# Performance work log

Measured on AMD Instinct MI355X. Metric: run time of the kernel, lower is better.

Reference implementation:

```python
import jax, jax.numpy as jnp
import numpy as np

# dims: B batch, T timesteps, S sensors, O obs_dim, E obs_embed_dim, P pe_emb_dim, A inter-sensor attn dim
B, T, S, O, E, P, A, OUT = 64, 128, 64, 4, 64, 16, 10, 128


def positional_encoding(times, pe_dim):
    # standard sinusoidal PE over continuous times -> (B, T, pe_dim)
    # (sin block then cos block; mathematically same frequencies as interleaved torch version)
    freq = jnp.exp(jnp.arange(0, pe_dim, 2, dtype=jnp.float32) * (-jnp.log(10000.0) / pe_dim))
    ang = times[..., None] * freq  # (B, T, pe_dim//2)
    return jnp.concatenate([jnp.sin(ang), jnp.cos(ang)], axis=-1)


def setup_inputs() -> dict:
    key = jax.random.key(0)
    ks = jax.random.split(key, 16)
    x = jax.random.normal(ks[0], (B, T, S, O), dtype=jnp.float32)
    times = jnp.sort(jax.random.uniform(ks[1], (B, T), dtype=jnp.float32) * 100.0, axis=1)
    mask = (jax.random.uniform(ks[2], (B, T, S), dtype=jnp.float32) < 0.8).astype(jnp.float32)
    s = 0.1  # param scale (module inits near zero; use small random for a meaningful baseline)
    params = dict(
        obs_emb_weights=jax.random.normal(ks[3], (S, O, E), dtype=jnp.float32) * s,
        inter_sensor_attn_weights=jax.random.normal(ks[4], (S, A), dtype=jnp.float32) * s,
        W_recv=jax.random.normal(ks[5], (E, A + P), dtype=jnp.float32) * s,
        b_recv=jax.random.normal(ks[6], (A + P,), dtype=jnp.float32) * s,
        bidir_weights=jax.random.normal(ks[7], (S, E), dtype=jnp.float32) * s,
        W_q=jax.random.normal(ks[8], (E + P, A), dtype=jnp.float32) * s,
        b_q=jax.random.normal(ks[9], (A,), dtype=jnp.float32) * s,
        W_k=jax.random.normal(ks[10], (E + P, A), dtype=jnp.float32) * s,
        b_k=jax.random.normal(ks[11], (A,), dtype=jnp.float32) * s,
        W_s=jax.random.normal(ks[12], (T, 1), dtype=jnp.float32) * s,
        b_s=jax.random.normal(ks[13], (1,), dtype=jnp.float32) * s,
        W_emb=jax.random.normal(ks[14], (E + P, OUT), dtype=jnp.float32) * s,
        b_emb=jax.random.normal(ks[15], (OUT,), dtype=jnp.float32) * s,
    )
    return dict(x=x, times=times, mask=mask, **params)


def reference(x, times, mask, obs_emb_weights, inter_sensor_attn_weights,
              W_recv, b_recv, bidir_weights, W_q, b_q, W_k, b_k,
              W_s, b_s, W_emb, b_emb):
    b, t, s, _ = x.shape
    e = obs_emb_weights.shape[-1]
    pe_dim = W_recv.shape[1] - inter_sensor_attn_weights.shape[1]

    # per-sensor observation embedding, masked
    h = jax.nn.relu(jnp.einsum('btso,soe->btse', x, obs_emb_weights))
    h = h * mask[..., None]

    pe = positional_encoding(times, pe_dim)                      # (B,T,P)
    pe_rep = jnp.broadcast_to(pe[:, :, None, :], (b, t, s, pe_dim))

    # inter-sensor attention alpha: (B,T,S_recv,S_send)
    attn_cat = jnp.concatenate(
        [jnp.broadcast_to(inter_sensor_attn_weights[None, None], (b, t, s, inter_sensor_attn_weights.shape[1])),
         pe_rep], axis=-1)                                        # (B,T,S,A+P)
    h_map = h @ W_recv + b_recv                                   # (B,T,S,A+P)
    alpha = jax.nn.relu(jnp.einsum('btid,btjd->btij', h_map, attn_cat))

    bidir = bidir_weights @ bidir_weights.T                       # (S,S)

    def propagate(h_in, adj):
        # fused form of: (h.unsqueeze(2) * (bidir*alpha*adj)[...,None]).sum(3)
        w = bidir[None, None] * alpha * adj[:, None]              # (B,T,S,S)
        return jax.nn.relu(jnp.einsum('btij,btje->btie', w, h_in))

    adj1 = jnp.ones((b, s, s), dtype=x.dtype)
    h = propagate(h, adj1)
    adj2 = adj1 * (alpha.sum(axis=1) / mask.sum(axis=1)[..., None])  # (B,S,S)
    h = propagate(h, adj2)

    H = jnp.concatenate([h, pe_rep], axis=-1).transpose(0, 2, 1, 3)  # (B,S,T,E+P)

    # temporal self-attention
    Q = H @ W_q + b_q                                             # (B,S,T,A)
    K = H @ W_k + b_k
    scale = 1.0 / jnp.sqrt(jnp.float32(e + pe_dim))
    beta = jnp.einsum('bsta,bsua->bstu', Q, K) * scale            # (B,S,T,T)
    beta = (beta @ W_s)[..., 0] + b_s[0]                          # (B,S,T)
    beta = jax.nn.softmax(beta, axis=-1)

    out = jnp.einsum('bst,bstd->bsd', beta, H) @ W_emb + b_emb    # (B,S,OUT)
    return out
```

## Files before the change

kernel.cpp:

```cpp
#include <hip/hip_runtime.h>
#include <hip/hip_bf16.h>


typedef unsigned short u16;
typedef unsigned int u32;
typedef __attribute__((ext_vector_type(8))) short short8;
typedef __attribute__((ext_vector_type(4))) float f32x4;

#define OFF_PE    0
#define OFF_BIDIR 131072
#define OFF_MS    135168
#define OFF_ADJ   139264
#define OFF_BRP   401408
#define OFF_ST    401424
#define BOFF_WRT  1638464u
#define BOFF_CATX 1642560u
#define BOFF_PEH  1644608u
#define BOFF_V    2431040u
#define BOFF_HH   3479616u

__device__ __forceinline__ u16 f2bf(float f){
  __hip_bfloat16 h = __float2bfloat16(f);
  union { __hip_bfloat16 h; u16 u; } v; v.h = h; return v.u;
}
__device__ __forceinline__ u32 pk2bf(float lo, float hi){
  __hip_bfloat162 h = __float22bfloat162_rn(float2{lo, hi});
  union { __hip_bfloat162 h; u32 u; } v; v.h = h; return v.u;
}
__device__ __forceinline__ float bf2f(u16 h){
  union { u32 u; float f; } v; v.u = ((u32)h) << 16; return v.f;
}

__global__ void k_pre(const float* __restrict__ times, const float* __restrict__ mask,
                      const float* __restrict__ Wb, const float* __restrict__ Wrecv,
                      const float* __restrict__ brecv, const float* __restrict__ battn,
                      float* __restrict__ ws_f, char* __restrict__ ws_b) {
  __shared__ float peL[32][17];
  __shared__ float wpe[64][17];
  __shared__ float pm[4][64];
  const int blk = blockIdx.x, tid = threadIdx.x;
  u16* wrt  = (u16*)(ws_b + BOFF_WRT);
  u16* catx = (u16*)(ws_b + BOFF_CATX);
  u16* peh  = (u16*)(ws_b + BOFF_PEH);
  u16* vv   = (u16*)(ws_b + BOFF_V);
  float* ST = ws_f + OFF_ST;
  if (blk < 256) {
    #pragma unroll
    for (int r = 0; r < 2; ++r) {
      int id = blk * 512 + r * 256 + tid;
      int bt = id >> 4, k = id & 15;
      float tv = times[bt];
      int kk = k & 7;
      float fr = expf(-(float)kk * 1.1512925465f);
      float ang = tv * fr;
      float v = (k < 8) ? sinf(ang) : cosf(ang);
      peh[id] = f2bf(v);
      peL[r*16 + (tid >> 4)][k] = v;
    }
    #pragma unroll
    for (int q = 0; q < 4; ++q) {
      int idx = q * 256 + tid;
      wpe[idx >> 4][idx & 15] = Wrecv[(idx >> 4)*26 + 10 + (idx & 15)];
    }
    __syncthreads();
    {
      int btl = tid >> 3, e0 = (tid & 7) * 8;
      float acc[8];
      #pragma unroll
      for (int i = 0; i < 8; ++i) acc[i] = 0.f;
      #pragma unroll
      for (int k = 0; k < 16; ++k) {
        float p = peL[btl][k];
        #pragma unroll
        for (int i = 0; i < 8; ++i) acc[i] += wpe[e0 + i][k] * p;
      }
      u32* dst = (u32*)&vv[(blk*32 + btl)*64 + e0];
      #pragma unroll
      for (int p = 0; p < 4; ++p) dst[p] = pk2bf(acc[2*p], acc[2*p+1]);
      if (tid < 32) {
        float s = 0.f;
        #pragma unroll
        for (int k = 0; k < 16; ++k) s += brecv[10 + k] * peL[tid][k];
        ST[blk*32 + tid] = s;
      }
    }
  } else if (blk < 260) {
    float* bidir = ws_f + OFF_BIDIR;
    int q = blk - 256;
    for (int rr = 0; rr < 4; ++rr) {
      int idx = (q*4 + rr) * 256 + tid;
      int i = idx >> 6, j = idx & 63;
      float acc = 0.f;
      for (int e = 0; e < 64; ++e) acc += Wb[i*64+e] * Wb[j*64+e];
      bidir[idx] = acc;
    }
  } else if (blk == 260) {
    for (int r = 0; r < 8; ++r) {
      int idx = r * 256 + tid;
      int d = idx >> 6, e = idx & 63;
      wrt[idx] = (d < 26) ? f2bf(Wrecv[e*26 + d]) : (u16)0;
    }
    if (tid < 16) ws_f[OFF_BRP + tid] = (tid < 10) ? brecv[tid] : 0.f;
    #pragma unroll
    for (int i = 0; i < 4; ++i) {
      int idx = i * 256 + tid;
      int j = idx >> 4, d = idx & 15;
      catx[idx] = (d < 10) ? f2bf(battn[j*10 + d]) : ((d == 10) ? f2bf(1.f) : (u16)0);
    }
  } else {
    int b = blk - 261;
    int i = tid & 63, q = tid >> 6;
    float s = 0.f;
    for (int t = q*32; t < q*32 + 32; ++t) s += mask[(b*128 + t)*64 + i];
    pm[q][i] = s;
    __syncthreads();
    if (tid < 64)
      (ws_f + OFF_MS)[b*64 + tid] =
          1.0f / (pm[0][tid] + pm[1][tid] + pm[2][tid] + pm[3][tid]);
  }
}

__global__ __launch_bounds__(256)
void k_adj(const float* __restrict__ x, const float* __restrict__ mask,
           const float* __restrict__ Wobs, float* __restrict__ ws_f,
           const char* __restrict__ ws_b) {
  __shared__ __align__(16) u16 hA[64][72];
  __shared__ __align__(16) u16 hmA[64][24];

  const int tid = threadIdx.x;
  const int b = blockIdx.y, tc = blockIdx.x;
  const int w = tid >> 6, l = tid & 63, lr = l & 15, lq = l >> 4, kb = lq * 8;
  const u16* wrt  = (const u16*)(ws_b + BOFF_WRT);
  const u16* catx = (const u16*)(ws_b + BOFF_CATX);
  const u16* vv   = (const u16*)(ws_b + BOFF_V);
  const float* brp = ws_f + OFF_BRP;
  const float* ST = ws_f + OFF_ST;
  float* adj = ws_f + OFF_ADJ;

  const short8 z8 = (short8){0,0,0,0,0,0,0,0};
  const bool lowk = (lq < 2);
  short8 w0 = z8, w1 = z8;
  if (lr < 10) {
    const u16* wr = wrt + lr * 64;
    w0 = *(const short8*)&wr[kb];
    w1 = *(const short8*)&wr[32 + kb];
  }
  short8 bc[4];
  #pragma unroll
  for (int n = 0; n < 4; ++n)
    bc[n] = lowk ? *(const short8*)&catx[(16*n + lr)*16 + lq*8] : z8;
  float4 bv = *(const float4*)&brp[lq*4];

  f32x4 asum[4];
  #pragma unroll
  for (int n = 0; n < 4; ++n) asum[n] = (f32x4){0.f,0.f,0.f,0.f};

  const int e4 = tid & 15, sg = tid >> 4;

  for (int tt = 0; tt < 8; ++tt) {
    int t = tc * 8 + tt;
    int base = b * 128 + t;
    short8 av0 = z8, av1 = z8;
    if (lr == 10) {
      av0 = *(const short8*)&vv[base*64 + kb];
      av1 = *(const short8*)&vv[base*64 + 32 + kb];
    }
    float st = ST[base];
    {
      float4 mk4 = *(const float4*)&mask[base*64 + sg*4];
      float mks[4] = {mk4.x, mk4.y, mk4.z, mk4.w};
      #pragma unroll
      for (int si = 0; si < 4; ++si) {
        int s = sg*4 + si;
        float4 xv = *(const float4*)&x[base*256 + s*4];
        float xo[4] = {xv.x, xv.y, xv.z, xv.w};
        float ax = 0.f, ay = 0.f, az = 0.f, aw = 0.f;
        #pragma unroll
        for (int o = 0; o < 4; ++o) {
          float4 wv = *(const float4*)&Wobs[(s*4+o)*64 + e4*4];
          ax += xo[o]*wv.x; ay += xo[o]*wv.y; az += xo[o]*wv.z; aw += xo[o]*wv.w;
        }
        float mk = mks[si];
        uint2 p;
        p.x = pk2bf(fmaxf(ax,0.f)*mk, fmaxf(ay,0.f)*mk);
        p.y = pk2bf(fmaxf(az,0.f)*mk, fmaxf(aw,0.f)*mk);
        *(uint2*)&hA[s][e4*4] = p;
      }
    }
    __syncthreads();
    {
      short8 a0 = (lr < 10) ? w0 : av0;
      short8 a1 = (lr < 10) ? w1 : av1;
      f32x4 acc = (f32x4){0.f,0.f,0.f,0.f};
      short8 b0 = *(const short8*)&hA[16*w + lr][kb];
      short8 b1 = *(const short8*)&hA[16*w + lr][32 + kb];
      acc = __builtin_amdgcn_mfma_f32_16x16x32_bf16(a0, b0, acc, 0, 0, 0);
      acc = __builtin_amdgcn_mfma_f32_16x16x32_bf16(a1, b1, acc, 0, 0, 0);
      uint2 qq;
      qq.x = pk2bf(acc[0]+bv.x, acc[1]+bv.y);
      qq.y = pk2bf(acc[2]+bv.z, acc[3]+bv.w);
      *(uint2*)&hmA[16*w + lr][lq*4] = qq;
    }
    __syncthreads();
    {
      short8 am = lowk ? *(const short8*)&hmA[16*w + lr][lq*8] : z8;
      #pragma unroll
      for (int n = 0; n < 4; ++n) {
        f32x4 z = (f32x4){st, st, st, st};
        z = __builtin_amdgcn_mfma_f32_16x16x32_bf16(am, bc[n], z, 0, 0, 0);
        #pragma unroll
        for (int reg = 0; reg < 4; ++reg) asum[n][reg] += fmaxf(z[reg], 0.f);
      }
    }
    __syncthreads();
  }
  #pragma unroll
  for (int n = 0; n < 4; ++n) {
    #pragma unroll
    for (int reg = 0; reg < 4; ++reg) {
      int i = 16*w + lq*4 + reg, j = 16*n + lr;
      atomicAdd(&adj[((size_t)b << 12) + (i << 6) + j], asum[n][reg]);
    }
  }
}

__global__ __launch_bounds__(256, 4)
void k_main(const float* __restrict__ x, const float* __restrict__ mask,
            const float* __restrict__ Wobs, const float* __restrict__ ws_f,
            const char* __restrict__ ws_b, u16* __restrict__ Hh) {
  __shared__ __align__(16) char smem[36864];
  u16 (*hA)[72]  = (u16 (*)[72])(smem);
  u16 (*hT)[72]  = (u16 (*)[72])(smem + 9216);
  u16 (*wA)[72]  = (u16 (*)[72])(smem + 18432);
  u16 (*hmA)[24] = (u16 (*)[24])(smem + 27648);
  u16 (*adjS)[72]= (u16 (*)[72])(smem + 27648);
  u16 (*h2L)[72] = (u16 (*)[72])(smem + 9216);

  const int tid = threadIdx.x;
  const int t = blockIdx.x, b = blockIdx.y;
  const int w = tid >> 6, l = tid & 63, lr = l & 15, lq = l >> 4, kb = lq * 8;
  const int base = b * 128 + t;
  const u16* wrt  = (const u16*)(ws_b + BOFF_WRT);
  const u16* catx = (const u16*)(ws_b + BOFF_CATX);
  const u16* vv   = (const u16*)(ws_b + BOFF_V);
  const float* bidirG = ws_f + OFF_BIDIR;
  const float* brp = ws_f + OFF_BRP;
  const float* msInv = ws_f + OFF_MS + b * 64;
  const int i0 = 16*w + lq*4;
  const short8 z8 = (short8){0,0,0,0,0,0,0,0};
  const bool lowk = (lq < 2);

  const float4* agf = (const float4*)(ws_f + OFF_ADJ + (size_t)b * 4096);
  float4 ga0 = agf[tid], ga1 = agf[tid + 256], ga2 = agf[tid + 512], ga3 = agf[tid + 768];
  float msr0 = msInv[(tid >> 4)], msr1 = msInv[(tid >> 4) + 16],
        msr2 = msInv[(tid >> 4) + 32], msr3 = msInv[(tid >> 4) + 48];
  short8 w0 = z8, w1 = z8;
  if (lr < 10) {
    const u16* wr = wrt + lr * 64;
    w0 = *(const short8*)&wr[kb];
    w1 = *(const short8*)&wr[32 + kb];
  }
  short8 av0 = z8, av1 = z8;
  if (lr == 10) {
    av0 = *(const short8*)&vv[base*64 + kb];
    av1 = *(const short8*)&vv[base*64 + 32 + kb];
  }
  short8 bc[4];
  #pragma unroll
  for (int n = 0; n < 4; ++n)
    bc[n] = lowk ? *(const short8*)&catx[(16*n + lr)*16 + lq*8] : z8;
  float4 bv = *(const float4*)&brp[lq*4];
  const float st = (ws_f + OFF_ST)[base];

  {
    const int e4 = tid & 15, sg = tid >> 4;
    float4 mk4 = *(const float4*)&mask[base*64 + sg*4];
    float mks[4] = {mk4.x, mk4.y, mk4.z, mk4.w};
    #pragma unroll
    for (int si = 0; si < 4; ++si) {
      int s = sg*4 + si;
      float4 xv = *(const float4*)&x[base*256 + s*4];
      float xo[4] = {xv.x, xv.y, xv.z, xv.w};
      float ax = 0.f, ay = 0.f, az = 0.f, aw = 0.f;
      #pragma unroll
      for (int o = 0; o < 4; ++o) {
        float4 wv = *(const float4*)&Wobs[(s*4+o)*64 + e4*4];
        ax += xo[o]*wv.x; ay += xo[o]*wv.y; az += xo[o]*wv.z; aw += xo[o]*wv.w;
      }
      float mk = mks[si];
      uint2 p;
      p.x = pk2bf(fmaxf(ax,0.f)*mk, fmaxf(ay,0.f)*mk);
      p.y = pk2bf(fmaxf(az,0.f)*mk, fmaxf(aw,0.f)*mk);
      *(uint2*)&hA[s][e4*4] = p;
    }
  }
  __syncthreads();

  {
    #pragma unroll
    for (int sp = 0; sp < 8; ++sp) {
      int s = w*16 + sp*2;
      *(u32*)&hT[l][s] = (u32)hA[s][l] | ((u32)hA[s+1][l] << 16);
    }
    short8 a0 = (lr < 10) ? w0 : av0;
    short8 a1 = (lr < 10) ? w1 : av1;
    f32x4 acc = (f32x4){0.f,0.f,0.f,0.f};
    short8 b0 = *(const short8*)&hA[16*w + lr][kb];
    short8 b1 = *(const short8*)&hA[16*w + lr][32 + kb];
    acc = __builtin_amdgcn_mfma_f32_16x16x32_bf16(a0, b0, acc, 0, 0, 0);
    acc = __builtin_amdgcn_mfma_f32_16x16x32_bf16(a1, b1, acc, 0, 0, 0);
    uint2 qq;
    qq.x = pk2bf(acc[0]+bv.x, acc[1]+bv.y);
    qq.y = pk2bf(acc[2]+bv.z, acc[3]+bv.w);
    *(uint2*)&hmA[16*w + lr][lq*4] = qq;
  }
  __syncthreads();

  {
    short8 am = lowk ? *(const short8*)&hmA[16*w + lr][lq*8] : z8;
    #pragma unroll
    for (int n = 0; n < 4; ++n) {
      f32x4 z = (f32x4){st, st, st, st};
      z = __builtin_amdgcn_mfma_f32_16x16x32_bf16(am, bc[n], z, 0, 0, 0);
      int j = 16*n + lr;
      #pragma unroll
      for (int reg = 0; reg < 4; ++reg) {
        float w1v = fmaxf(z[reg], 0.f) * bidirG[((i0+reg) << 6) + j];
        wA[i0 + reg][j] = f2bf(w1v);
      }
    }
  }
  __syncthreads();

  {
    int arow = tid >> 4, acol = (tid & 15) * 4;
    uint2 p;
    p.x = pk2bf(ga0.x*msr0, ga0.y*msr0); p.y = pk2bf(ga0.z*msr0, ga0.w*msr0);
    *(uint2*)&adjS[arow][acol] = p;
    p.x = pk2bf(ga1.x*msr1, ga1.y*msr1); p.y = pk2bf(ga1.z*msr1, ga1.w*msr1);
    *(uint2*)&adjS[arow + 16][acol] = p;
    p.x = pk2bf(ga2.x*msr2, ga2.y*msr2); p.y = pk2bf(ga2.z*msr2, ga2.w*msr2);
    *(uint2*)&adjS[arow + 32][acol] = p;
    p.x = pk2bf(ga3.x*msr3, ga3.y*msr3); p.y = pk2bf(ga3.z*msr3, ga3.w*msr3);
    *(uint2*)&adjS[arow + 48][acol] = p;

    short8 aw0 = *(const short8*)&wA[16*w + lr][kb];
    short8 aw1 = *(const short8*)&wA[16*w + lr][32 + kb];
    #pragma unroll
    for (int n = 0; n < 4; ++n) {
      f32x4 acc = (f32x4){0.f,0.f,0.f,0.f};
      short8 b0 = *(const short8*)&hT[16*n + lr][kb];
      short8 b1 = *(const short8*)&hT[16*n + lr][32 + kb];
      acc = __builtin_amdgcn_mfma_f32_16x16x32_bf16(aw0, b0, acc, 0, 0, 0);
      acc = __builtin_amdgcn_mfma_f32_16x16x32_bf16(aw1, b1, acc, 0, 0, 0);
      int e = 16*n + lr;
      uint2 pp;
      pp.x = pk2bf(fmaxf(acc[0],0.f), fmaxf(acc[1],0.f));
      pp.y = pk2bf(fmaxf(acc[2],0.f), fmaxf(acc[3],0.f));
      *(uint2*)&hA[e][i0] = pp;
    }
  }
  __syncthreads();

  {
    int row = 16*w + lr;
    union { short8 v; u16 h[8]; u32 u[4]; } uw0, uw1, ud0, ud1, oa, ob;
    uw0.v = *(const short8*)&wA[row][kb];
    uw1.v = *(const short8*)&wA[row][32 + kb];
    ud0.v = *(const short8*)&adjS[row][kb];
    ud1.v = *(const short8*)&adjS[row][32 + kb];
    #pragma unroll
    for (int k = 0; k < 4; ++k) {
      oa.u[k] = pk2bf(bf2f(uw0.h[2*k])*bf2f(ud0.h[2*k]),
                      bf2f(uw0.h[2*k+1])*bf2f(ud0.h[2*k+1]));
      ob.u[k] = pk2bf(bf2f(uw1.h[2*k])*bf2f(ud1.h[2*k]),
                      bf2f(uw1.h[2*k+1])*bf2f(ud1.h[2*k+1]));
    }
    short8 a20 = oa.v, a21 = ob.v;
    #pragma unroll
    for (int n = 0; n < 4; ++n) {
      f32x4 acc = (f32x4){0.f,0.f,0.f,0.f};
      short8 b0 = *(const short8*)&hA[16*n + lr][kb];
      short8 b1 = *(const short8*)&hA[16*n + lr][32 + kb];
      acc = __builtin_amdgcn_mfma_f32_16x16x32_bf16(a20, b0, acc, 0, 0, 0);
      acc = __builtin_amdgcn_mfma_f32_16x16x32_bf16(a21, b1, acc, 0, 0, 0);
      int e = 16*n + lr;
      u32 p0 = pk2bf(fmaxf(acc[0],0.f), fmaxf(acc[1],0.f));
      u32 p1 = pk2bf(fmaxf(acc[2],0.f), fmaxf(acc[3],0.f));
      h2L[i0+0][e] = (u16)p0;
      h2L[i0+1][e] = (u16)(p0 >> 16);
      h2L[i0+2][e] = (u16)p1;
      h2L[i0+3][e] = (u16)(p1 >> 16);
    }
  }
  __syncthreads();

  {
    int i = tid >> 2, q = tid & 3;
    const uint4* srcv = (const uint4*)&h2L[i][q * 16];
    uint4 v0 = srcv[0], v1 = srcv[1];
    size_t obase = ((size_t)b * 64) * 8192 + (size_t)t * 64;
    uint4* dst = (uint4*)&Hh[obase + (size_t)i * 8192 + q * 16];
    dst[0] = v0; dst[1] = v1;
  }
}

#define HTP 82

__global__ __launch_bounds__(512)
void k_attn(const char* __restrict__ ws_b, const u16* __restrict__ Hh,
            const float* __restrict__ Wq, const float* __restrict__ bq,
            const float* __restrict__ Wk, const float* __restrict__ bk,
            const float* __restrict__ Ws, const float* __restrict__ bs,
            const float* __restrict__ Wemb, const float* __restrict__ bemb,
            float* __restrict__ out) {
  __shared__ u16 Ht[128][HTP];
  __shared__ u16 peB[128][18];
  __shared__ float wsL[128];
  __shared__ float pA[6][80];
  __shared__ float pK[8][10];
  __shared__ float qvL[80];
  __shared__ float pC[4][128];
  __shared__ float bb[128];
  __shared__ float red[4];
  __shared__ float cstL, sWL;

  const int tid = threadIdx.x;
  const int s = blockIdx.x, b = blockIdx.y;
  const float scale = 0.111803398875f;
  const u16* peh = (const u16*)(ws_b + BOFF_PEH);

  const u16* src = Hh + ((size_t)b * 64 + s) * 8192;
  #pragma unroll
  for (int r = 0; r < 2; ++r) {
    int id = r * 512 + tid;
    int tt = id >> 3, c = (id & 7) * 8;
    uint4 q = *(const uint4*)&src[tt * 64 + c];
    u32* dst = (u32*)&Ht[tt][c];
    dst[0] = q.x; dst[1] = q.y; dst[2] = q.z; dst[3] = q.w;
  }
  #pragma unroll
  for (int r = 0; r < 2; ++r) {
    int id = r * 512 + tid;
    u32 pv = ((const u32*)(peh + (size_t)b * 2048))[id];
    *(u32*)&peB[id >> 3][(id & 7) * 2] = pv;
  }
  if (tid < 128) wsL[tid] = Ws[tid];
  __syncthreads();

  if (tid < 480) {
    int d = tid % 80, c = tid / 80;
    int t0 = c * 22, t1 = (t0 + 22 > 128) ? 128 : t0 + 22;
    float a0 = 0.f, a1 = 0.f, a2 = 0.f, a3 = 0.f;
    int t = t0;
    if (d < 64) {
      for (; t + 4 <= t1; t += 4) {
        a0 += wsL[t]   * bf2f(Ht[t][d]);
        a1 += wsL[t+1] * bf2f(Ht[t+1][d]);
        a2 += wsL[t+2] * bf2f(Ht[t+2][d]);
        a3 += wsL[t+3] * bf2f(Ht[t+3][d]);
      }
      for (; t < t1; ++t) a0 += wsL[t] * bf2f(Ht[t][d]);
    } else {
      int k = d - 64;
      for (; t + 4 <= t1; t += 4) {
        a0 += wsL[t]   * bf2f(peB[t][k]);
        a1 += wsL[t+1] * bf2f(peB[t+1][k]);
        a2 += wsL[t+2] * bf2f(peB[t+2][k]);
        a3 += wsL[t+3] * bf2f(peB[t+3][k]);
      }
      for (; t < t1; ++t) a0 += wsL[t] * bf2f(peB[t][k]);
    }
    pA[c][d] = (a0 + a1) + (a2 + a3);
  } else if (tid == 480) {
    float a0 = 0.f, a1 = 0.f, a2 = 0.f, a3 = 0.f;
    for (int t = 0; t < 128; t += 4) {
      a0 += wsL[t]; a1 += wsL[t+1]; a2 += wsL[t+2]; a3 += wsL[t+3];
    }
    sWL = (a0 + a1) + (a2 + a3);
  }
  __syncthreads();

  if (tid < 80) {
    int a = tid % 10, c = tid / 10;
    float a0 = 0.f, a1 = 0.f;
    #pragma unroll
    for (int i = 0; i < 10; i += 2) {
      int d = c * 10 + i;
      float h0 = pA[0][d] + pA[1][d] + pA[2][d] + pA[3][d] + pA[4][d] + pA[5][d];
      float h1 = pA[0][d+1] + pA[1][d+1] + pA[2][d+1] + pA[3][d+1] + pA[4][d+1] + pA[5][d+1];
      a0 += h0 * Wk[d * 10 + a];
      a1 += h1 * Wk[(d+1) * 10 + a];
    }
    pK[c][a] = a0 + a1;
  }
  __syncthreads();

  if (tid <= 80) {
    float kt[10];
    #pragma unroll
    for (int a = 0; a < 10; ++a) {
      float acc = sWL * bk[a];
      #pragma unroll
      for (int c = 0; c < 8; ++c) acc += pK[c][a];
      kt[a] = acc;
    }
    if (tid < 80) {
      float a0 = 0.f, a1 = 0.f;
      #pragma unroll
      for (int a = 0; a < 10; a += 2) {
        a0 += Wq[tid * 10 + a] * kt[a];
        a1 += Wq[tid * 10 + a + 1] * kt[a + 1];
      }
      qvL[tid] = a0 + a1;
    } else {
      float cq = 0.f;
      #pragma unroll
      for (int a = 0; a < 10; ++a) cq += bq[a] * kt[a];
      cstL = scale * cq + bs[0];
    }
  }
  __syncthreads();

  {
    int t = tid & 127, q = tid >> 7;
    float a0 = 0.f, a1 = 0.f, a2 = 0.f, a3 = 0.f;
    const u32* row = (const u32*)&Ht[t][0];
    if (q == 0) {
      #pragma unroll
      for (int i = 0; i < 10; i += 2) {
        u32 p0 = row[i], p1 = row[i+1];
        a0 += bf2f((u16)p0) * qvL[2*i]   + bf2f((u16)(p0 >> 16)) * qvL[2*i+1];
        a1 += bf2f((u16)p1) * qvL[2*i+2] + bf2f((u16)(p1 >> 16)) * qvL[2*i+3];
      }
    } else if (q == 1) {
      #pragma unroll
      for (int i = 10; i < 20; i += 2) {
        u32 p0 = row[i], p1 = row[i+1];
        a0 += bf2f((u16)p0) * qvL[2*i]   + bf2f((u16)(p0 >> 16)) * qvL[2*i+1];
        a1 += bf2f((u16)p1) * qvL[2*i+2] + bf2f((u16)(p1 >> 16)) * qvL[2*i+3];
      }
    } else if (q == 2) {
      #pragma unroll
      for (int i = 20; i < 32; i += 4) {
        u32 p0 = row[i], p1 = row[i+1], p2 = row[i+2], p3 = row[i+3];
        a0 += bf2f((u16)p0) * qvL[2*i]   + bf2f((u16)(p0 >> 16)) * qvL[2*i+1];
        a1 += bf2f((u16)p1) * qvL[2*i+2] + bf2f((u16)(p1 >> 16)) * qvL[2*i+3];
        a2 += bf2f((u16)p2) * qvL[2*i+4] + bf2f((u16)(p2 >> 16)) * qvL[2*i+5];
        a3 += bf2f((u16)p3) * qvL[2*i+6] + bf2f((u16)(p3 >> 16)) * qvL[2*i+7];
      }
    } else {
      #pragma unroll
      for (int k = 0; k < 16; k += 4) {
        a0 += bf2f(peB[t][k])   * qvL[64 + k];
        a1 += bf2f(peB[t][k+1]) * qvL[65 + k];
        a2 += bf2f(peB[t][k+2]) * qvL[66 + k];
        a3 += bf2f(peB[t][k+3]) * qvL[67 + k];
      }
    }
    pC[q][t] = (a0 + a1) + (a2 + a3);
  }
  __syncthreads();

  if (tid < 128) {
    float v = scale * (pC[0][tid] + pC[1][tid] + pC[2][tid] + pC[3][tid]) + cstL;
    bb[tid] = v;
    float mm = v;
    #pragma unroll
    for (int off = 32; off; off >>= 1) mm = fmaxf(mm, __shfl_xor(mm, off));
    if ((tid & 63) == 0) red[tid >> 6] = mm;
  }
  __syncthreads();
  float mx = fmaxf(red[0], red[1]);
  if (tid < 128) {
    float ev = expf(bb[tid] - mx);
    bb[tid] = ev;
    float ss = ev;
    #pragma unroll
    for (int off = 32; off; off >>= 1) ss += __shfl_xor(ss, off);
    if ((tid & 63) == 0) red[2 + (tid >> 6)] = ss;
  }
  __syncthreads();

  if (tid < 480) {
    int d = tid % 80, c = tid / 80;
    int t0 = c * 22, t1 = (t0 + 22 > 128) ? 128 : t0 + 22;
    float a0 = 0.f, a1 = 0.f, a2 = 0.f, a3 = 0.f;
    int t = t0;
    if (d < 64) {
      for (; t + 4 <= t1; t += 4) {
        a0 += bb[t]   * bf2f(Ht[t][d]);
        a1 += bb[t+1] * bf2f(Ht[t+1][d]);
        a2 += bb[t+2] * bf2f(Ht[t+2][d]);
        a3 += bb[t+3] * bf2f(Ht[t+3][d]);
      }
      for (; t < t1; ++t) a0 += bb[t] * bf2f(Ht[t][d]);
    } else {
      int k = d - 64;
      for (; t + 4 <= t1; t += 4) {
        a0 += bb[t]   * bf2f(peB[t][k]);
        a1 += bb[t+1] * bf2f(peB[t+1][k]);
        a2 += bb[t+2] * bf2f(peB[t+2][k]);
        a3 += bb[t+3] * bf2f(peB[t+3][k]);
      }
      for (; t < t1; ++t) a0 += bb[t] * bf2f(peB[t][k]);
    }
    pA[c][d] = (a0 + a1) + (a2 + a3);
  }
  __syncthreads();

  {
    int o = tid & 127, q = tid >> 7;
    int d0 = q * 20;
    float a0 = 0.f, a1 = 0.f, a2 = 0.f, a3 = 0.f;
    #pragma unroll
    for (int i = 0; i < 20; i += 4) {
      int d = d0 + i;
      float h0 = pA[0][d]   + pA[1][d]   + pA[2][d]   + pA[3][d]   + pA[4][d]   + pA[5][d];
      float h1 = pA[0][d+1] + pA[1][d+1] + pA[2][d+1] + pA[3][d+1] + pA[4][d+1] + pA[5][d+1];
      float h2 = pA[0][d+2] + pA[1][d+2] + pA[2][d+2] + pA[3][d+2] + pA[4][d+2] + pA[5][d+2];
      float h3 = pA[0][d+3] + pA[1][d+3] + pA[2][d+3] + pA[3][d+3] + pA[4][d+3] + pA[5][d+3];
      a0 += h0 * Wemb[d * 128 + o];
      a1 += h1 * Wemb[(d+1) * 128 + o];
      a2 += h2 * Wemb[(d+2) * 128 + o];
      a3 += h3 * Wemb[(d+3) * 128 + o];
    }
    pC[q][o] = (a0 + a1) + (a2 + a3);
  }
  __syncthreads();
  if (tid < 128) {
    float rdenom = 1.0f / (red[2] + red[3]);
    out[(((size_t)b * 64 + s) << 7) + tid] =
        bemb[tid] + (pC[0][tid] + pC[1][tid] + pC[2][tid] + pC[3][tid]) * rdenom;
  }
}

extern "C" void kernel_launch(void* const* d_in, const int* in_sizes, int n_in,
                              void* d_out, int out_size, void* d_ws, size_t ws_size,
                              hipStream_t stream) {
  (void)in_sizes; (void)n_in; (void)out_size; (void)ws_size;
  const float* x     = (const float*)d_in[0];
  const float* times = (const float*)d_in[1];
  const float* mask  = (const float*)d_in[2];
  const float* Wobs  = (const float*)d_in[3];
  const float* Wattn = (const float*)d_in[4];
  const float* Wrecv = (const float*)d_in[5];
  const float* brecv = (const float*)d_in[6];
  const float* Wb    = (const float*)d_in[7];
  const float* Wq    = (const float*)d_in[8];
  const float* bq    = (const float*)d_in[9];
  const float* Wk    = (const float*)d_in[10];
  const float* bk    = (const float*)d_in[11];
  const float* Ws    = (const float*)d_in[12];
  const float* bs    = (const float*)d_in[13];
  const float* Wemb  = (const float*)d_in[14];
  const float* bemb  = (const float*)d_in[15];
  float* out = (float*)d_out;
  float* ws_f = (float*)d_ws;
  char* ws_b = (char*)d_ws;
  u16* Hh = (u16*)(ws_b + BOFF_HH);

  hipMemsetAsync(ws_b + (size_t)OFF_ADJ * 4, 0, (size_t)64 * 64 * 64 * 4, stream);
  k_pre<<<325, 256, 0, stream>>>(times, mask, Wb, Wrecv, brecv, Wattn, ws_f, ws_b);
  k_adj<<<dim3(16, 64), 256, 0, stream>>>(x, mask, Wobs, ws_f, ws_b);
  k_main<<<dim3(128, 64), 256, 0, stream>>>(x, mask, Wobs, ws_f, ws_b, Hh);
  k_attn<<<dim3(64, 64), 512, 0, stream>>>(ws_b, Hh, Wq, bq, Wk, bk, Ws, bs, Wemb, bemb, out);
}
```

Before: 161.3 us.

## Precompute scaled bf16 adjacency in separate kernel and write Hh directly

Adds a small k_scale kernel that multiplies each batch's adjacency by the inverse mask sums and stores it as bf16 once. k_main then loads that bf16 block instead of the fp32 adjacency plus per-row scale for each of the 128 timestep blocks, halving that global read and removing the conversion work. It also drops the final LDS staging pass and __syncthreads, writing Hh with scattered 2-byte global stores instead of coalesced 16-byte ones. The cost is an extra kernel launch and a less coalesced output write pattern.

```diff
diff --git a/kernel.cpp b/kernel.cpp
--- a/kernel.cpp
+++ b/kernel.cpp
@@ -7,7 +7,6 @@
 typedef __attribute__((ext_vector_type(8))) short short8;
 typedef __attribute__((ext_vector_type(4))) float f32x4;
 
-#define OFF_PE    0
 #define OFF_BIDIR 131072
 #define OFF_MS    135168
 #define OFF_ADJ   139264
@@ -16,6 +15,7 @@
 #define BOFF_WRT  1638464u
 #define BOFF_CATX 1642560u
 #define BOFF_PEH  1644608u
+#define BOFF_ADJS 1906752u
 #define BOFF_V    2431040u
 #define BOFF_HH   3479616u
 
@@ -224,6 +224,20 @@
   }
 }
 
+__global__ __launch_bounds__(256)
+void k_scale(const float* __restrict__ ws_f, char* __restrict__ ws_b) {
+  const int b = blockIdx.x, tid = threadIdx.x;
+  const float* adj = ws_f + OFF_ADJ + (size_t)b * 4096;
+  const float* msI = ws_f + OFF_MS + b * 64;
+  u16* as_ = (u16*)(ws_b + BOFF_ADJS) + (size_t)b * 4096;
+  #pragma unroll
+  for (int k = 0; k < 16; ++k) {
+    int idx = k * 256 + tid;
+    int i = idx >> 6;
+    as_[idx] = f2bf(adj[idx] * msI[i]);
+  }
+}
+
 __global__ __launch_bounds__(256, 4)
 void k_main(const float* __restrict__ x, const float* __restrict__ mask,
             const float* __restrict__ Wobs, const float* __restrict__ ws_f,
@@ -234,7 +248,6 @@
   u16 (*wA)[72]  = (u16 (*)[72])(smem + 18432);
   u16 (*hmA)[24] = (u16 (*)[24])(smem + 27648);
   u16 (*adjS)[72]= (u16 (*)[72])(smem + 27648);
-  u16 (*h2L)[72] = (u16 (*)[72])(smem + 9216);
 
   const int tid = threadIdx.x;
   const int t = blockIdx.x, b = blockIdx.y;
@@ -245,15 +258,12 @@
   const u16* vv   = (const u16*)(ws_b + BOFF_V);
   const float* bidirG = ws_f + OFF_BIDIR;
   const float* brp = ws_f + OFF_BRP;
-  const float* msInv = ws_f + OFF_MS + b * 64;
   const int i0 = 16*w + lq*4;
   const short8 z8 = (short8){0,0,0,0,0,0,0,0};
   const bool lowk = (lq < 2);
 
-  const float4* agf = (const float4*)(ws_f + OFF_ADJ + (size_t)b * 4096);
-  float4 ga0 = agf[tid], ga1 = agf[tid + 256], ga2 = agf[tid + 512], ga3 = agf[tid + 768];
-  float msr0 = msInv[(tid >> 4)], msr1 = msInv[(tid >> 4) + 16],
-        msr2 = msInv[(tid >> 4) + 32], msr3 = msInv[(tid >> 4) + 48];
+  const uint4* ag = (const uint4*)(ws_b + BOFF_ADJS + (size_t)b * 8192);
+  uint4 g0 = ag[2*tid], g1 = ag[2*tid + 1];
   short8 w0 = z8, w1 = z8;
   if (lr < 10) {
     const u16* wr = wrt + lr * 64;
@@ -333,16 +343,9 @@
   __syncthreads();
 
   {
-    int arow = tid >> 4, acol = (tid & 15) * 4;
-    uint2 p;
-    p.x = pk2bf(ga0.x*msr0, ga0.y*msr0); p.y = pk2bf(ga0.z*msr0, ga0.w*msr0);
-    *(uint2*)&adjS[arow][acol] = p;
-    p.x = pk2bf(ga1.x*msr1, ga1.y*msr1); p.y = pk2bf(ga1.z*msr1, ga1.w*msr1);
-    *(uint2*)&adjS[arow + 16][acol] = p;
-    p.x = pk2bf(ga2.x*msr2, ga2.y*msr2); p.y = pk2bf(ga2.z*msr2, ga2.w*msr2);
-    *(uint2*)&adjS[arow + 32][acol] = p;
-    p.x = pk2bf(ga3.x*msr3, ga3.y*msr3); p.y = pk2bf(ga3.z*msr3, ga3.w*msr3);
-    *(uint2*)&adjS[arow + 48][acol] = p;
+    int idx0 = 2*tid, idx1 = 2*tid + 1;
+    *(uint4*)&adjS[idx0 >> 3][(idx0 & 7) * 8] = g0;
+    *(uint4*)&adjS[idx1 >> 3][(idx1 & 7) * 8] = g1;
 
     short8 aw0 = *(const short8*)&wA[16*w + lr][kb];
     short8 aw1 = *(const short8*)&wA[16*w + lr][32 + kb];
@@ -377,6 +380,7 @@
                       bf2f(uw1.h[2*k+1])*bf2f(ud1.h[2*k+1]));
     }
     short8 a20 = oa.v, a21 = ob.v;
+    size_t obase = ((size_t)b * 64) * 8192 + (size_t)t * 64;
     #pragma unroll
     for (int n = 0; n < 4; ++n) {
       f32x4 acc = (f32x4){0.f,0.f,0.f,0.f};
@@ -387,21 +391,11 @@
       int e = 16*n + lr;
       u32 p0 = pk2bf(fmaxf(acc[0],0.f), fmaxf(acc[1],0.f));
       u32 p1 = pk2bf(fmaxf(acc[2],0.f), fmaxf(acc[3],0.f));
-      h2L[i0+0][e] = (u16)p0;
-      h2L[i0+1][e] = (u16)(p0 >> 16);
-      h2L[i0+2][e] = (u16)p1;
-      h2L[i0+3][e] = (u16)(p1 >> 16);
-    }
-  }
-  __syncthreads();
-
-  {
-    int i = tid >> 2, q = tid & 3;
-    const uint4* srcv = (const uint4*)&h2L[i][q * 16];
-    uint4 v0 = srcv[0], v1 = srcv[1];
-    size_t obase = ((size_t)b * 64) * 8192 + (size_t)t * 64;
-    uint4* dst = (uint4*)&Hh[obase + (size_t)i * 8192 + q * 16];
-    dst[0] = v0; dst[1] = v1;
+      Hh[obase + (size_t)(i0+0) * 8192 + e] = (u16)p0;
+      Hh[obase + (size_t)(i0+1) * 8192 + e] = (u16)(p0 >> 16);
+      Hh[obase + (size_t)(i0+2) * 8192 + e] = (u16)p1;
+      Hh[obase + (size_t)(i0+3) * 8192 + e] = (u16)(p1 >> 16);
+    }
   }
 }
 
@@ -663,6 +657,7 @@
   hipMemsetAsync(ws_b + (size_t)OFF_ADJ * 4, 0, (size_t)64 * 64 * 64 * 4, stream);
   k_pre<<<325, 256, 0, stream>>>(times, mask, Wb, Wrecv, brecv, Wattn, ws_f, ws_b);
   k_adj<<<dim3(16, 64), 256, 0, stream>>>(x, mask, Wobs, ws_f, ws_b);
+  k_scale<<<64, 256, 0, stream>>>(ws_f, ws_b);
   k_main<<<dim3(128, 64), 256, 0, stream>>>(x, mask, Wobs, ws_f, ws_b, Hh);
   k_attn<<<dim3(64, 64), 512, 0, stream>>>(ws_b, Hh, Wq, bq, Wk, bk, Ws, bs, Wemb, bemb, out);
 }
```

New measurement: 149.9 us. 7.1% less time.
